# Performance work log

Measured on AMD Instinct MI355X. Metric: run time of the kernel, lower is better.

Reference implementation:

```python
import jax, jax.numpy as jnp
import numpy as np

B, P = 4, 2048
NUM_MODS, D_TIME = 22, 8
DIM_S = NUM_MODS + D_TIME + 1          # 31
PHI_W, PSI_W, PSI_LAT = 32, 32, 32
DOT, HEADS, RHO_W = 16, 4, 64


def _xavier(key, shape):
    fan_in, fan_out = shape[0], shape[1]
    std = (2.0 / (fan_in + fan_out)) ** 0.5
    return jax.random.normal(key, shape, jnp.float32) * std


def setup_inputs() -> dict:
    key = jax.random.key(0)
    ks = jax.random.split(key, 20)
    inp = {
        "times": jnp.sort(jax.random.uniform(ks[0], (B, P), jnp.float32) * 100.0, axis=1),
        "values": jax.random.normal(ks[1], (B, P), jnp.float32),
        "measurements": jax.random.randint(ks[2], (B, P), 0, NUM_MODS + 1, jnp.int64 if jax.config.jax_enable_x64 else jnp.int32),
        "non_pad_mask": jnp.ones((B, P, 1), jnp.float32),
        # attention.psi MLP_state(dim_s -> psi_width)
        "psi_w1": _xavier(ks[3], (DIM_S, PSI_W)), "psi_b1": jnp.zeros((PSI_W,), jnp.float32),
        "psi_w2": _xavier(ks[4], (PSI_W, PSI_W)), "psi_b2": jnp.zeros((PSI_W,), jnp.float32),
        # attention.rho Linear(psi_width -> psi_latent_width)
        "arho_w": _xavier(ks[5], (PSI_W, PSI_LAT)), "arho_b": jnp.zeros((PSI_LAT,), jnp.float32),
        # attention key/query projections
        "W_k": _xavier(ks[6], (PSI_LAT + DIM_S, DOT * HEADS)),
        "W_q": _xavier(ks[7], (HEADS, DOT)),
        # phi MLP_state(dim_s -> phi_width)
        "phi_w1": _xavier(ks[8], (DIM_S, PHI_W)), "phi_b1": jnp.zeros((PHI_W,), jnp.float32),
        "phi_w2": _xavier(ks[9], (PHI_W, PHI_W)), "phi_b2": jnp.zeros((PHI_W,), jnp.float32),
        # rho MLP_state(n_heads*phi_width -> rho_width)
        "rho_w1": _xavier(ks[10], (HEADS * PHI_W, RHO_W)), "rho_b1": jnp.zeros((RHO_W,), jnp.float32),
        "rho_w2": _xavier(ks[11], (RHO_W, RHO_W)), "rho_b2": jnp.zeros((RHO_W,), jnp.float32),
    }
    return inp


def _mlp_state(x, mask, w1, b1, w2, b2):
    # MLP_state: relu(fc1(x*mask)); relu(fc2(h*mask)); h*mask  (dropout p=0)
    h = jax.nn.relu((x * mask) @ w1 + b1)
    h = jax.nn.relu((h * mask) @ w2 + b2)
    return h * mask


def _forward(times, values, measurements, non_pad_mask,
             psi_w1, psi_b1, psi_w2, psi_b2, arho_w, arho_b, W_k, W_q,
             phi_w1, phi_b1, phi_w2, phi_b2, rho_w1, rho_b1, rho_w2, rho_b2):
    mask = non_pad_mask  # [B,P,1]
    # temporal encoding: time / 10000^(2*(i//2)/d_time), sin on even, cos on odd
    idx = jnp.arange(D_TIME)
    pos_vec = jnp.power(10000.0, 2.0 * (idx // 2).astype(jnp.float32) / D_TIME)
    r = times[:, :, None] / pos_vec[None, None, :]          # [B,P,d_time]
    tenc = jnp.where(idx % 2 == 0, jnp.sin(r), jnp.cos(r))
    # one-hot measurements, drop padding channel 0
    meas = jax.nn.one_hot(measurements, NUM_MODS + 1, dtype=jnp.float32)[:, :, 1:]
    combined = jnp.concatenate([tenc, values[:, :, None], meas], axis=-1)  # [B,P,dim_s]

    # --- CumulativeSetAttentionLayer ---
    enc_psi = _mlp_state(combined, mask, psi_w1, psi_b1, psi_w2, psi_b2)   # [B,P,psi_w]
    counts = jnp.arange(1, P + 1, dtype=jnp.float32)[None, :, None]
    agg = jnp.cumsum(enc_psi, axis=1) / counts * mask                      # cumulative mean
    agg = (agg @ arho_w + arho_b) * mask                                   # [B,P,psi_lat]
    comb2 = jnp.concatenate([combined, agg], axis=-1)                      # [B,P,dim_s+psi_lat]
    keys = (comb2 @ W_k) * mask                                            # [B,P,DOT*HEADS]
    # torch.split(keys, n_heads, -1) + stack(-1): chunk i has size HEADS -> [B,P,HEADS,DOT]
    keys = keys.reshape(B, P, DOT, HEADS).transpose(0, 1, 3, 2)            # [B,P,h,d]
    preattn = jnp.einsum('bphd,hd->bph', keys, W_q) / jnp.sqrt(jnp.float32(DOT))
    preattn = preattn * mask                                               # [B,P,m]

    # --- phi encoding ---
    enc = _mlp_state(combined, mask, phi_w1, phi_b1, phi_w2, phi_b2)       # [B,P,d_phi]

    # --- cumulative causal softmax weighting ---
    A = preattn[:, None, :, :]                                             # [B,1,Q,m]
    Bc = jax.lax.cummax(preattn, axis=1)[:, :, None, :]                    # [B,P,1,m]
    triu = jnp.triu(jnp.ones((P, P), bool), 1)[None, :, :, None]           # mask Q > P
    D = jnp.exp(jnp.where(triu, -jnp.inf, A - Bc))                          # [B,P,Q,m]
    E = jnp.sum(D, axis=2)                                                 # [B,P,m]
    out5 = jnp.einsum('bpqm,bqd->bpmd', D, enc) / E[:, :, :, None]
    out5 = out5 * mask[:, :, :, None]                                      # [B,P,m,d_phi]

    agg2 = out5.reshape(B, P, HEADS * PHI_W)
    output = _mlp_state(agg2, mask, rho_w1, rho_b1, rho_w2, rho_b2)        # [B,P,rho_w]
    return output


def reference(times, values, measurements, non_pad_mask,
              psi_w1, psi_b1, psi_w2, psi_b2, arho_w, arho_b, W_k, W_q,
              phi_w1, phi_b1, phi_w2, phi_b2, rho_w1, rho_b1, rho_w2, rho_b2):
    return _forward(times, values, measurements, non_pad_mask,
                    psi_w1, psi_b1, psi_w2, psi_b2, arho_w, arho_b, W_k, W_q,
                    phi_w1, phi_b1, phi_w2, phi_b2, rho_w1, rho_b1, rho_w2, rho_b2)
```

## Files before the change

### kernel.cpp

```cpp
#include <hip/hip_runtime.h>
#include <math.h>

#define PB 2048
#define OFF_PSI 262144
#define OFF_ENC 524288
#define OFF_PRE 786432
#define OFF_WV  819200

__global__ __launch_bounds__(64) void k_encode(
    const float* __restrict__ times, const float* __restrict__ vals,
    const int* __restrict__ meas, const float* __restrict__ mask,
    const float* __restrict__ psi_w1, const float* __restrict__ psi_b1,
    const float* __restrict__ psi_w2, const float* __restrict__ psi_b2,
    const float* __restrict__ phi_w1, const float* __restrict__ phi_b1,
    const float* __restrict__ phi_w2, const float* __restrict__ phi_b2,
    float* __restrict__ ws)
{
    __shared__ float sW[4222];
    for (int i = threadIdx.x; i < 1023; i += 64) {
        int r = i / 33, cc = i - r * 33;
        sW[i]        = (cc < 32) ? psi_w1[r*32 + cc] : 0.0f;
        sW[2111 + i] = (cc < 32) ? phi_w1[r*32 + cc] : 0.0f;
    }
    for (int i = threadIdx.x; i < 1024; i += 64) {
        sW[1055 + i] = psi_w2[i];
        sW[3166 + i] = phi_w2[i];
    }
    if (threadIdx.x < 32) {
        int i = threadIdx.x;
        sW[1023 + i] = psi_b1[i];
        sW[2079 + i] = psi_b2[i];
        sW[3134 + i] = phi_b1[i];
        sW[4190 + i] = phi_b2[i];
    }
    __syncthreads();

    const int pp = blockIdx.x * 64 + threadIdx.x;
    const int b = pp >> 11, p = pp & 2047;
    const float t = times[pp];
    const float v = vals[pp];
    const float msk = mask[pp];
    const int m = meas[pp];

    float c[9];
    c[0] = sinf(t);           c[1] = cosf(t);
    c[2] = sinf(t * 0.1f);    c[3] = cosf(t * 0.1f);
    c[4] = sinf(t * 0.01f);   c[5] = cosf(t * 0.01f);
    c[6] = sinf(t * 0.001f);  c[7] = cosf(t * 0.001f);
    c[8] = v;

    float* comb_t = ws;
    float* psi_t  = ws + OFF_PSI;
    float* enc_t  = ws + OFF_ENC;
    const int cb = b * 32;

    #pragma unroll
    for (int i = 0; i < 8; i++) comb_t[(cb + i) * PB + p] = c[i];
    comb_t[(cb + 8) * PB + p] = v;
    #pragma unroll
    for (int k = 9; k < 31; k++)
        comb_t[(cb + k) * PB + p] = (k == 8 + m) ? 1.0f : 0.0f;
    comb_t[(cb + 31) * PB + p] = msk;

    float x[9];
    #pragma unroll
    for (int i = 0; i < 9; i++) x[i] = c[i] * msk;
    const float ohs = (m > 0) ? msk : 0.0f;
    const int   ohr = (m > 0) ? (8 + m) * 33 : 0;

    {
        float h1[32];
        #pragma unroll
        for (int j = 0; j < 32; j++) {
            float acc = sW[1023 + j];
            #pragma unroll
            for (int i = 0; i < 9; i++) acc = fmaf(x[i], sW[i*33 + j], acc);
            acc = fmaf(ohs, sW[ohr + j], acc);
            h1[j] = fmaxf(acc, 0.0f) * msk;
        }
        #pragma unroll
        for (int j = 0; j < 32; j++) {
            float acc = sW[2079 + j];
            #pragma unroll
            for (int i = 0; i < 32; i++) acc = fmaf(h1[i], sW[1055 + i*32 + j], acc);
            psi_t[(cb + j) * PB + p] = fmaxf(acc, 0.0f) * msk;
        }
    }
    {
        float h1[32];
        #pragma unroll
        for (int j = 0; j < 32; j++) {
            float acc = sW[3134 + j];
            #pragma unroll
            for (int i = 0; i < 9; i++) acc = fmaf(x[i], sW[2111 + i*33 + j], acc);
            acc = fmaf(ohs, sW[2111 + ohr + j], acc);
            h1[j] = fmaxf(acc, 0.0f) * msk;
        }
        #pragma unroll
        for (int j = 0; j < 32; j++) {
            float acc = sW[4190 + j];
            #pragma unroll
            for (int i = 0; i < 32; i++) acc = fmaf(h1[i], sW[3166 + i*32 + j], acc);
            enc_t[(cb + j) * PB + p] = fmaxf(acc, 0.0f) * msk;
        }
    }
}

__global__ __launch_bounds__(64) void k_scan(float* __restrict__ data)
{
    float* base = data + (size_t)blockIdx.x * PB;
    const int lane = threadIdx.x;
    float v[32];
    float4* b4 = (float4*)(base + lane * 32);
    #pragma unroll
    for (int k = 0; k < 8; k++) {
        float4 f = b4[k];
        v[4*k] = f.x; v[4*k+1] = f.y; v[4*k+2] = f.z; v[4*k+3] = f.w;
    }
    #pragma unroll
    for (int j = 1; j < 32; j++) v[j] += v[j-1];
    const float tot = v[31];
    float x = tot;
    #pragma unroll
    for (int off = 1; off < 64; off <<= 1) {
        float y = __shfl_up(x, off);
        if (lane >= off) x += y;
    }
    const float excl = x - tot;
    #pragma unroll
    for (int j = 0; j < 32; j++) v[j] += excl;
    #pragma unroll
    for (int k = 0; k < 8; k++)
        b4[k] = make_float4(v[4*k], v[4*k+1], v[4*k+2], v[4*k+3]);
}

__global__ __launch_bounds__(64) void k_attnpre(
    const float* __restrict__ arho_w, const float* __restrict__ arho_b,
    const float* __restrict__ W_k, const float* __restrict__ W_q,
    float* __restrict__ ws)
{
    __shared__ float sU[31*4];
    __shared__ float sU2[32*4];
    __shared__ float sV[32*4];
    __shared__ float sC[4];
    for (int t = threadIdx.x; t < 252; t += 64) {
        int i = t >> 2, h = t & 3;
        float s = 0.0f;
        #pragma unroll
        for (int d = 0; d < 16; d++)
            s = fmaf(W_k[i*64 + d*4 + h], W_q[h*16 + d], s);
        s *= 0.25f;
        if (i < 31) sU[i*4 + h] = s; else sU2[(i-31)*4 + h] = s;
    }
    __syncthreads();
    for (int t = threadIdx.x; t < 128; t += 64) {
        int ch = t >> 2, h = t & 3;
        float s = 0.0f;
        #pragma unroll
        for (int j = 0; j < 32; j++)
            s = fmaf(arho_w[ch*32 + j], sU2[j*4 + h], s);
        sV[t] = s;
    }
    if (threadIdx.x < 4) {
        float s = 0.0f;
        #pragma unroll
        for (int j = 0; j < 32; j++)
            s = fmaf(arho_b[j], sU2[j*4 + threadIdx.x], s);
        sC[threadIdx.x] = s;
    }
    __syncthreads();

    const int pp = blockIdx.x * 64 + threadIdx.x;
    const int b = pp >> 11, p = pp & 2047;
    const float* comb_t = ws;
    const float* psi_t  = ws + OFF_PSI;
    float* pre = ws + OFF_PRE;
    const int cb = b * 32;
    const float msk = comb_t[(size_t)(cb + 31) * PB + p];
    const float inv = msk / (float)(p + 1);

    float pr[4] = {sC[0], sC[1], sC[2], sC[3]};
    #pragma unroll
    for (int i = 0; i < 31; i++) {
        const float ci = comb_t[(size_t)(cb + i) * PB + p];
        #pragma unroll
        for (int h = 0; h < 4; h++) pr[h] = fmaf(ci, sU[i*4 + h], pr[h]);
    }
    #pragma unroll
    for (int ch = 0; ch < 32; ch++) {
        const float ag = psi_t[(size_t)(cb + ch) * PB + p] * inv;
        #pragma unroll
        for (int h = 0; h < 4; h++) pr[h] = fmaf(ag, sV[ch*4 + h], pr[h]);
    }
    #pragma unroll
    for (int h = 0; h < 4; h++)
        pre[(size_t)(b*4 + h) * PB + p] = expf(pr[h] * msk);
}

__global__ __launch_bounds__(64) void k_scan2w(float* __restrict__ ws)
{
    const int blk = blockIdx.x;
    const int bh = blk / 33;
    const int c  = blk - bh * 33;
    const int b  = bh >> 2;
    const int lane = threadIdx.x;

    const float4* s4 = (const float4*)(ws + OFF_PRE + (size_t)bh * PB + lane * 32);
    const float4* e4 = (const float4*)(ws + OFF_ENC + ((size_t)(b*32 + (c-1))) * PB + lane * 32);
    float4* o4 = (float4*)(ws + OFF_WV + ((size_t)(bh*33 + c)) * PB + lane * 32);

    float v[32];
    #pragma unroll
    for (int k = 0; k < 8; k++) {
        float4 f = s4[k];
        v[4*k] = f.x; v[4*k+1] = f.y; v[4*k+2] = f.z; v[4*k+3] = f.w;
    }
    if (c > 0) {
        #pragma unroll
        for (int k = 0; k < 8; k++) {
            float4 f = e4[k];
            v[4*k] *= f.x; v[4*k+1] *= f.y; v[4*k+2] *= f.z; v[4*k+3] *= f.w;
        }
    }
    #pragma unroll
    for (int j = 1; j < 32; j++) v[j] += v[j-1];
    const float tot = v[31];
    float x = tot;
    #pragma unroll
    for (int off = 1; off < 64; off <<= 1) {
        float y = __shfl_up(x, off);
        if (lane >= off) x += y;
    }
    const float excl = x - tot;
    #pragma unroll
    for (int j = 0; j < 32; j++) v[j] += excl;
    #pragma unroll
    for (int k = 0; k < 8; k++)
        o4[k] = make_float4(v[4*k], v[4*k+1], v[4*k+2], v[4*k+3]);
}

__global__ __launch_bounds__(256) void k_rho(
    const float* __restrict__ rho_w1, const float* __restrict__ rho_b1,
    const float* __restrict__ rho_w2, const float* __restrict__ rho_b2,
    const float* __restrict__ ws, float* __restrict__ out)
{
    __shared__ float h1s[16][65];
    __shared__ float scl[16][4];
    __shared__ float mskS[16];
    const int tid = threadIdx.x;
    const int pos = tid >> 4;
    const int g   = tid & 15;
    const int pbase = blockIdx.x * 16;
    const int b  = pbase >> 11;
    const int p0 = pbase & 2047;
    const float* wv = ws + OFF_WV + (size_t)b * 132 * PB;

    if (tid < 64) {
        const int pp = tid >> 2, h = tid & 3;
        const float msk = ws[(size_t)(b*32 + 31) * PB + p0 + pp];
        const float L = wv[(size_t)(h*33) * PB + p0 + pp];
        scl[pp][h] = msk / L;
        if (h == 0) mskS[pp] = msk;
    }
    __syncthreads();

    const int pg = p0 + pos;
    float4 acc = ((const float4*)rho_b1)[g];
    const float4* w14 = (const float4*)rho_w1;
    const float sc0 = scl[pos][0], sc1 = scl[pos][1];
    const float sc2 = scl[pos][2], sc3 = scl[pos][3];
    #pragma unroll
    for (int h = 0; h < 4; h++) {
        const float sc = (h == 0) ? sc0 : (h == 1) ? sc1 : (h == 2) ? sc2 : sc3;
        const float* wvh = wv + (size_t)(h*33 + 1) * PB + pg;
        #pragma unroll 8
        for (int d = 0; d < 32; d++) {
            const float ai = wvh[(size_t)d * PB] * sc;
            const float4 w = w14[(h*32 + d)*16 + g];
            acc.x = fmaf(ai, w.x, acc.x);
            acc.y = fmaf(ai, w.y, acc.y);
            acc.z = fmaf(ai, w.z, acc.z);
            acc.w = fmaf(ai, w.w, acc.w);
        }
    }
    const float msk = mskS[pos];
    h1s[pos][g*4+0] = fmaxf(acc.x, 0.f) * msk;
    h1s[pos][g*4+1] = fmaxf(acc.y, 0.f) * msk;
    h1s[pos][g*4+2] = fmaxf(acc.z, 0.f) * msk;
    h1s[pos][g*4+3] = fmaxf(acc.w, 0.f) * msk;
    __syncthreads();

    float4 acc2 = ((const float4*)rho_b2)[g];
    const float4* w24 = (const float4*)rho_w2;
    #pragma unroll 16
    for (int i = 0; i < 64; i++) {
        const float hv = h1s[pos][i];
        const float4 w = w24[i*16 + g];
        acc2.x = fmaf(hv, w.x, acc2.x);
        acc2.y = fmaf(hv, w.y, acc2.y);
        acc2.z = fmaf(hv, w.z, acc2.z);
        acc2.w = fmaf(hv, w.w, acc2.w);
    }
    float4 o;
    o.x = fmaxf(acc2.x, 0.f) * msk;
    o.y = fmaxf(acc2.y, 0.f) * msk;
    o.z = fmaxf(acc2.z, 0.f) * msk;
    o.w = fmaxf(acc2.w, 0.f) * msk;
    ((float4*)out)[(size_t)(pbase + pos) * 16 + g] = o;
}

extern "C" void kernel_launch(void* const* d_in, const int* in_sizes, int n_in,
                              void* d_out, int out_size, void* d_ws, size_t ws_size,
                              hipStream_t stream)
{
    const float* times  = (const float*)d_in[0];
    const float* vals   = (const float*)d_in[1];
    const int*   meas   = (const int*)d_in[2];
    const float* mask   = (const float*)d_in[3];
    const float* psi_w1 = (const float*)d_in[4];
    const float* psi_b1 = (const float*)d_in[5];
    const float* psi_w2 = (const float*)d_in[6];
    const float* psi_b2 = (const float*)d_in[7];
    const float* arho_w = (const float*)d_in[8];
    const float* arho_b = (const float*)d_in[9];
    const float* W_k    = (const float*)d_in[10];
    const float* W_q    = (const float*)d_in[11];
    const float* phi_w1 = (const float*)d_in[12];
    const float* phi_b1 = (const float*)d_in[13];
    const float* phi_w2 = (const float*)d_in[14];
    const float* phi_b2 = (const float*)d_in[15];
    const float* rho_w1 = (const float*)d_in[16];
    const float* rho_b1 = (const float*)d_in[17];
    const float* rho_w2 = (const float*)d_in[18];
    const float* rho_b2 = (const float*)d_in[19];
    float* ws  = (float*)d_ws;
    float* out = (float*)d_out;

    k_encode<<<dim3(128), dim3(64), 0, stream>>>(times, vals, meas, mask,
        psi_w1, psi_b1, psi_w2, psi_b2, phi_w1, phi_b1, phi_w2, phi_b2, ws);
    k_scan<<<dim3(128), dim3(64), 0, stream>>>(ws + OFF_PSI);
    k_attnpre<<<dim3(128), dim3(64), 0, stream>>>(arho_w, arho_b, W_k, W_q, ws);
    k_scan2w<<<dim3(528), dim3(64), 0, stream>>>(ws);
    k_rho<<<dim3(512), dim3(256), 0, stream>>>(rho_w1, rho_b1, rho_w2, rho_b2, ws, out);
}
```

Before: 146.4 us.

## Project psi onto per-head scores before scanning, fusing attention prep into encode

Uses linearity of the cumulative mean: instead of scanning all 32 psi channels and then projecting, the encode kernel projects psi to 4 per-head values q and computes the static per-position score r. Only q gets scanned; the scan is folded into the middle kernel, which rebuilds the exp pre-attention on the fly. This removes two kernel launches and the 32-channel comb/psi write and read traffic. The cost is a redundant 4-head scan inside each of the 33 blocks per head and some extra weight-prep work in every encode block.

```diff
diff --git a/kernel.cpp b/kernel.cpp
--- a/kernel.cpp
+++ b/kernel.cpp
@@ -2,10 +2,11 @@
 #include <math.h>
 
 #define PB 2048
-#define OFF_PSI 262144
-#define OFF_ENC 524288
-#define OFF_PRE 786432
-#define OFF_WV  819200
+#define OFF_ENC 0
+#define OFF_Q   262144
+#define OFF_R   294912
+#define OFF_MSK 327680
+#define OFF_WV  335872
 
 __global__ __launch_bounds__(64) void k_encode(
     const float* __restrict__ times, const float* __restrict__ vals,
@@ -14,9 +15,15 @@
     const float* __restrict__ psi_w2, const float* __restrict__ psi_b2,
     const float* __restrict__ phi_w1, const float* __restrict__ phi_b1,
     const float* __restrict__ phi_w2, const float* __restrict__ phi_b2,
+    const float* __restrict__ arho_w, const float* __restrict__ arho_b,
+    const float* __restrict__ W_k, const float* __restrict__ W_q,
     float* __restrict__ ws)
 {
     __shared__ float sW[4222];
+    __shared__ float sU[31*4];
+    __shared__ float sU2[32*4];
+    __shared__ float sV[32*4];
+    __shared__ float sCc[4];
     for (int i = threadIdx.x; i < 1023; i += 64) {
         int r = i / 33, cc = i - r * 33;
         sW[i]        = (cc < 32) ? psi_w1[r*32 + cc] : 0.0f;
@@ -33,6 +40,31 @@
         sW[3134 + i] = phi_b1[i];
         sW[4190 + i] = phi_b2[i];
     }
+    for (int t = threadIdx.x; t < 252; t += 64) {
+        int i = t >> 2, h = t & 3;
+        float s = 0.0f;
+        #pragma unroll
+        for (int d = 0; d < 16; d++)
+            s = fmaf(W_k[i*64 + d*4 + h], W_q[h*16 + d], s);
+        s *= 0.25f;
+        if (i < 31) sU[i*4 + h] = s; else sU2[(i-31)*4 + h] = s;
+    }
+    __syncthreads();
+    for (int t = threadIdx.x; t < 128; t += 64) {
+        int ch = t >> 2, h = t & 3;
+        float s = 0.0f;
+        #pragma unroll
+        for (int j = 0; j < 32; j++)
+            s = fmaf(arho_w[ch*32 + j], sU2[j*4 + h], s);
+        sV[t] = s;
+    }
+    if (threadIdx.x < 4) {
+        float s = 0.0f;
+        #pragma unroll
+        for (int j = 0; j < 32; j++)
+            s = fmaf(arho_b[j], sU2[j*4 + threadIdx.x], s);
+        sCc[threadIdx.x] = s;
+    }
     __syncthreads();
 
     const int pp = blockIdx.x * 64 + threadIdx.x;
@@ -49,18 +81,8 @@
     c[6] = sinf(t * 0.001f);  c[7] = cosf(t * 0.001f);
     c[8] = v;
 
-    float* comb_t = ws;
-    float* psi_t  = ws + OFF_PSI;
-    float* enc_t  = ws + OFF_ENC;
+    float* enc_t = ws + OFF_ENC;
     const int cb = b * 32;
-
-    #pragma unroll
-    for (int i = 0; i < 8; i++) comb_t[(cb + i) * PB + p] = c[i];
-    comb_t[(cb + 8) * PB + p] = v;
-    #pragma unroll
-    for (int k = 9; k < 31; k++)
-        comb_t[(cb + k) * PB + p] = (k == 8 + m) ? 1.0f : 0.0f;
-    comb_t[(cb + 31) * PB + p] = msk;
 
     float x[9];
     #pragma unroll
@@ -68,6 +90,21 @@
     const float ohs = (m > 0) ? msk : 0.0f;
     const int   ohr = (m > 0) ? (8 + m) * 33 : 0;
 
+    float r[4] = {sCc[0], sCc[1], sCc[2], sCc[3]};
+    #pragma unroll
+    for (int i = 0; i < 9; i++) {
+        #pragma unroll
+        for (int h = 0; h < 4; h++) r[h] = fmaf(c[i], sU[i*4 + h], r[h]);
+    }
+    if (m > 0) {
+        #pragma unroll
+        for (int h = 0; h < 4; h++) r[h] += sU[(8 + m)*4 + h];
+    }
+    #pragma unroll
+    for (int h = 0; h < 4; h++)
+        ws[OFF_R + (size_t)(b*4 + h) * PB + p] = r[h];
+    ws[OFF_MSK + (size_t)b * PB + p] = msk;
+
     {
         float h1[32];
         #pragma unroll
@@ -78,13 +115,19 @@
             acc = fmaf(ohs, sW[ohr + j], acc);
             h1[j] = fmaxf(acc, 0.0f) * msk;
         }
+        float q[4] = {0.f, 0.f, 0.f, 0.f};
         #pragma unroll
         for (int j = 0; j < 32; j++) {
             float acc = sW[2079 + j];
             #pragma unroll
             for (int i = 0; i < 32; i++) acc = fmaf(h1[i], sW[1055 + i*32 + j], acc);
-            psi_t[(cb + j) * PB + p] = fmaxf(acc, 0.0f) * msk;
-        }
+            const float p2 = fmaxf(acc, 0.0f) * msk;
+            #pragma unroll
+            for (int h = 0; h < 4; h++) q[h] = fmaf(p2, sV[j*4 + h], q[h]);
+        }
+        #pragma unroll
+        for (int h = 0; h < 4; h++)
+            ws[OFF_Q + (size_t)(b*4 + h) * PB + p] = q[h];
     }
     {
         float h1[32];
@@ -101,103 +144,12 @@
             float acc = sW[4190 + j];
             #pragma unroll
             for (int i = 0; i < 32; i++) acc = fmaf(h1[i], sW[3166 + i*32 + j], acc);
-            enc_t[(cb + j) * PB + p] = fmaxf(acc, 0.0f) * msk;
+            enc_t[(size_t)(cb + j) * PB + p] = fmaxf(acc, 0.0f) * msk;
         }
     }
 }
 
-__global__ __launch_bounds__(64) void k_scan(float* __restrict__ data)
-{
-    float* base = data + (size_t)blockIdx.x * PB;
-    const int lane = threadIdx.x;
-    float v[32];
-    float4* b4 = (float4*)(base + lane * 32);
-    #pragma unroll
-    for (int k = 0; k < 8; k++) {
-        float4 f = b4[k];
-        v[4*k] = f.x; v[4*k+1] = f.y; v[4*k+2] = f.z; v[4*k+3] = f.w;
-    }
-    #pragma unroll
-    for (int j = 1; j < 32; j++) v[j] += v[j-1];
-    const float tot = v[31];
-    float x = tot;
-    #pragma unroll
-    for (int off = 1; off < 64; off <<= 1) {
-        float y = __shfl_up(x, off);
-        if (lane >= off) x += y;
-    }
-    const float excl = x - tot;
-    #pragma unroll
-    for (int j = 0; j < 32; j++) v[j] += excl;
-    #pragma unroll
-    for (int k = 0; k < 8; k++)
-        b4[k] = make_float4(v[4*k], v[4*k+1], v[4*k+2], v[4*k+3]);
-}
-
-__global__ __launch_bounds__(64) void k_attnpre(
-    const float* __restrict__ arho_w, const float* __restrict__ arho_b,
-    const float* __restrict__ W_k, const float* __restrict__ W_q,
-    float* __restrict__ ws)
-{
-    __shared__ float sU[31*4];
-    __shared__ float sU2[32*4];
-    __shared__ float sV[32*4];
-    __shared__ float sC[4];
-    for (int t = threadIdx.x; t < 252; t += 64) {
-        int i = t >> 2, h = t & 3;
-        float s = 0.0f;
-        #pragma unroll
-        for (int d = 0; d < 16; d++)
-            s = fmaf(W_k[i*64 + d*4 + h], W_q[h*16 + d], s);
-        s *= 0.25f;
-        if (i < 31) sU[i*4 + h] = s; else sU2[(i-31)*4 + h] = s;
-    }
-    __syncthreads();
-    for (int t = threadIdx.x; t < 128; t += 64) {
-        int ch = t >> 2, h = t & 3;
-        float s = 0.0f;
-        #pragma unroll
-        for (int j = 0; j < 32; j++)
-            s = fmaf(arho_w[ch*32 + j], sU2[j*4 + h], s);
-        sV[t] = s;
-    }
-    if (threadIdx.x < 4) {
-        float s = 0.0f;
-        #pragma unroll
-        for (int j = 0; j < 32; j++)
-            s = fmaf(arho_b[j], sU2[j*4 + threadIdx.x], s);
-        sC[threadIdx.x] = s;
-    }
-    __syncthreads();
-
-    const int pp = blockIdx.x * 64 + threadIdx.x;
-    const int b = pp >> 11, p = pp & 2047;
-    const float* comb_t = ws;
-    const float* psi_t  = ws + OFF_PSI;
-    float* pre = ws + OFF_PRE;
-    const int cb = b * 32;
-    const float msk = comb_t[(size_t)(cb + 31) * PB + p];
-    const float inv = msk / (float)(p + 1);
-
-    float pr[4] = {sC[0], sC[1], sC[2], sC[3]};
-    #pragma unroll
-    for (int i = 0; i < 31; i++) {
-        const float ci = comb_t[(size_t)(cb + i) * PB + p];
-        #pragma unroll
-        for (int h = 0; h < 4; h++) pr[h] = fmaf(ci, sU[i*4 + h], pr[h]);
-    }
-    #pragma unroll
-    for (int ch = 0; ch < 32; ch++) {
-        const float ag = psi_t[(size_t)(cb + ch) * PB + p] * inv;
-        #pragma unroll
-        for (int h = 0; h < 4; h++) pr[h] = fmaf(ag, sV[ch*4 + h], pr[h]);
-    }
-    #pragma unroll
-    for (int h = 0; h < 4; h++)
-        pre[(size_t)(b*4 + h) * PB + p] = expf(pr[h] * msk);
-}
-
-__global__ __launch_bounds__(64) void k_scan2w(float* __restrict__ ws)
+__global__ __launch_bounds__(64) void k_mid(float* __restrict__ ws)
 {
     const int blk = blockIdx.x;
     const int bh = blk / 33;
@@ -205,15 +157,42 @@
     const int b  = bh >> 2;
     const int lane = threadIdx.x;
 
-    const float4* s4 = (const float4*)(ws + OFF_PRE + (size_t)bh * PB + lane * 32);
+    const float4* q4 = (const float4*)(ws + OFF_Q   + (size_t)bh * PB + lane * 32);
+    const float4* r4 = (const float4*)(ws + OFF_R   + (size_t)bh * PB + lane * 32);
+    const float4* m4 = (const float4*)(ws + OFF_MSK + (size_t)b  * PB + lane * 32);
     const float4* e4 = (const float4*)(ws + OFF_ENC + ((size_t)(b*32 + (c-1))) * PB + lane * 32);
     float4* o4 = (float4*)(ws + OFF_WV + ((size_t)(bh*33 + c)) * PB + lane * 32);
 
+    float vq[32];
+    #pragma unroll
+    for (int k = 0; k < 8; k++) {
+        float4 f = q4[k];
+        vq[4*k] = f.x; vq[4*k+1] = f.y; vq[4*k+2] = f.z; vq[4*k+3] = f.w;
+    }
+    #pragma unroll
+    for (int j = 1; j < 32; j++) vq[j] += vq[j-1];
+    {
+        const float tot = vq[31];
+        float x = tot;
+        #pragma unroll
+        for (int off = 1; off < 64; off <<= 1) {
+            float y = __shfl_up(x, off);
+            if (lane >= off) x += y;
+        }
+        const float excl = x - tot;
+        #pragma unroll
+        for (int j = 0; j < 32; j++) vq[j] += excl;
+    }
     float v[32];
     #pragma unroll
     for (int k = 0; k < 8; k++) {
-        float4 f = s4[k];
-        v[4*k] = f.x; v[4*k+1] = f.y; v[4*k+2] = f.z; v[4*k+3] = f.w;
+        const float4 fr = r4[k];
+        const float4 fm = m4[k];
+        const int p0 = lane * 32 + 4*k;
+        v[4*k+0] = expf(fm.x * (fr.x + vq[4*k+0] / (float)(p0 + 1)));
+        v[4*k+1] = expf(fm.y * (fr.y + vq[4*k+1] / (float)(p0 + 2)));
+        v[4*k+2] = expf(fm.z * (fr.z + vq[4*k+2] / (float)(p0 + 3)));
+        v[4*k+3] = expf(fm.w * (fr.w + vq[4*k+3] / (float)(p0 + 4)));
     }
     if (c > 0) {
         #pragma unroll
@@ -257,7 +236,7 @@
 
     if (tid < 64) {
         const int pp = tid >> 2, h = tid & 3;
-        const float msk = ws[(size_t)(b*32 + 31) * PB + p0 + pp];
+        const float msk = ws[OFF_MSK + (size_t)b * PB + p0 + pp];
         const float L = wv[(size_t)(h*33) * PB + p0 + pp];
         scl[pp][h] = msk / L;
         if (h == 0) mskS[pp] = msk;
@@ -337,9 +316,8 @@
     float* out = (float*)d_out;
 
     k_encode<<<dim3(128), dim3(64), 0, stream>>>(times, vals, meas, mask,
-        psi_w1, psi_b1, psi_w2, psi_b2, phi_w1, phi_b1, phi_w2, phi_b2, ws);
-    k_scan<<<dim3(128), dim3(64), 0, stream>>>(ws + OFF_PSI);
-    k_attnpre<<<dim3(128), dim3(64), 0, stream>>>(arho_w, arho_b, W_k, W_q, ws);
-    k_scan2w<<<dim3(528), dim3(64), 0, stream>>>(ws);
+        psi_w1, psi_b1, psi_w2, psi_b2, phi_w1, phi_b1, phi_w2, phi_b2,
+        arho_w, arho_b, W_k, W_q, ws);
+    k_mid<<<dim3(528), dim3(64), 0, stream>>>(ws);
     k_rho<<<dim3(512), dim3(256), 0, stream>>>(rho_w1, rho_b1, rho_w2, rho_b2, ws, out);
 }
```

Measured after the change: 139.9 us. 4.5% less time.
